# Kernel optimization log

Hardware: AMD Instinct MI355X
Metric: run time of the kernel (lower is better)

Reference implementation:

```python
import jax, jax.numpy as jnp
import numpy as np

VOCAB, EMBED, HIDDEN, N_CLASSES = 50257, 128, 256, 2
B = S = 512  # must be equal: the original module only runs when x.size(0)==x.size(1)


def gru_layer(x_seq, Wih, Whh, bih, bhh):
    """PyTorch-equation GRU over time axis 0. x_seq: (T, N, E) -> (T, N, H)."""
    T, N, _ = x_seq.shape
    H = Whh.shape[1]
    xi = x_seq @ Wih.T + bih  # precompute input projections for all steps: (T, N, 3H)

    def step(h, xi_t):
        gh = h @ Whh.T + bhh
        xr, xz, xn = jnp.split(xi_t, 3, axis=-1)
        hr, hz, hn = jnp.split(gh, 3, axis=-1)
        r = jax.nn.sigmoid(xr + hr)
        z = jax.nn.sigmoid(xz + hz)
        n = jnp.tanh(xn + r * hn)
        h_new = (1.0 - z) * n + z * h
        return h_new, h_new

    h0 = jnp.zeros((N, H), dtype=x_seq.dtype)
    _, ys = jax.lax.scan(step, h0, xi)
    return ys


def setup_inputs() -> dict:
    key = jax.random.key(0)
    ks = jax.random.split(key, 12)
    sc = 0.05
    return {
        "x": jax.random.randint(ks[0], (B, S), 0, VOCAB),
        "embed_table": jax.random.normal(ks[1], (VOCAB, EMBED), jnp.float32) * sc,
        "Wih0": jax.random.normal(ks[2], (3 * HIDDEN, EMBED), jnp.float32) * sc,
        "Whh0": jax.random.normal(ks[3], (3 * HIDDEN, HIDDEN), jnp.float32) * sc,
        "bih0": jax.random.normal(ks[4], (3 * HIDDEN,), jnp.float32) * sc,
        "bhh0": jax.random.normal(ks[5], (3 * HIDDEN,), jnp.float32) * sc,
        "Wih1": jax.random.normal(ks[6], (3 * HIDDEN, HIDDEN), jnp.float32) * sc,
        "Whh1": jax.random.normal(ks[7], (3 * HIDDEN, HIDDEN), jnp.float32) * sc,
        "bih1": jax.random.normal(ks[8], (3 * HIDDEN,), jnp.float32) * sc,
        "bhh1": jax.random.normal(ks[9], (3 * HIDDEN,), jnp.float32) * sc,
        "W_out": jax.random.normal(ks[10], (N_CLASSES, HIDDEN), jnp.float32) * sc,
        "b_out": jax.random.normal(ks[11], (N_CLASSES,), jnp.float32) * sc,
    }


def reference(x, embed_table, Wih0, Whh0, bih0, bhh0, Wih1, Whh1, bih1, bhh1, W_out, b_out):
    emb = embed_table[x]                 # (B, S, E)
    # nn.GRU default batch_first=False: dim 0 (=B) is TIME, dim 1 (=S) is batch.
    y = gru_layer(emb, Wih0, Whh0, bih0, bhh0)   # (B, S, H)
    y = gru_layer(y, Wih1, Whh1, bih1, bhh1)     # (B, S, H)
    h_t = y[:, -1, :]                    # (B, H)
    # self.dropout(h_t) in the original discards its result -> no-op.
    logit = h_t @ W_out.T + b_out        # (B, n_classes)
    return logit
```

## Files before the change

kernel.cpp:

```cpp
#include <hip/hip_runtime.h>
#include <hip/hip_fp16.h>

typedef _Float16 f16x2 __attribute__((ext_vector_type(2)));
typedef _Float16 half8 __attribute__((ext_vector_type(8)));

#define TS  512
#define HID 256
#define G3  768
#define EMB 128
#define NB1 8
#define RPB 96
#define CTL 767
#define BSZ 8

__device__ __forceinline__ float sigmoidf_(float x){ return 1.0f/(1.0f+__expf(-x)); }
__device__ __forceinline__ float tanhf_(float x){
  float e = __expf(-2.0f*fabsf(x));
  float t = (1.0f-e)/(1.0f+e);
  return copysignf(t,x);
}

__global__ __launch_bounds__(256) void xi0_kernel(const int* __restrict__ x,
    const float* __restrict__ emb_tab, const float* __restrict__ Wih0,
    const float* __restrict__ bih0, float* __restrict__ xi0)
{
  __shared__ float embs[8][EMB];
  __shared__ int idx8[8];
  int tid = threadIdx.x;
  int t0  = blockIdx.x * 8;
  if (tid < 8) idx8[tid] = x[(t0 + tid)*512 + 511];
  __syncthreads();
  for (int i = tid; i < 8*EMB; i += 256){
    int q = i >> 7, r = i & 127;
    embs[q][r] = emb_tab[(long)idx8[q]*EMB + r];
  }
  __syncthreads();
  for (int g = 0; g < 3; g++){
    int j = g*256 + tid;
    float b = bih0[j];
    float acc[8];
    #pragma unroll
    for (int u=0;u<8;u++) acc[u]=b;
    const float4* wrow = (const float4*)(Wih0 + (long)j*EMB);
    #pragma unroll 8
    for (int m=0;m<EMB/4;m++){
      float4 w = wrow[m];
      #pragma unroll
      for (int u=0;u<8;u++){
        acc[u] += w.x*embs[u][4*m+0] + w.y*embs[u][4*m+1]
                + w.z*embs[u][4*m+2] + w.w*embs[u][4*m+3];
      }
    }
    #pragma unroll
    for (int u=0;u<8;u++) xi0[(long)(t0+u)*G3 + j] = acc[u];
  }
}

#define SHUF(V,A,B) __builtin_shufflevector(V,V,A,B)
#define WR32(X) X(0,0) X(0,1) X(0,2) X(0,3) X(1,0) X(1,1) X(1,2) X(1,3) \
                X(2,0) X(2,1) X(2,2) X(2,3) X(3,0) X(3,1) X(3,2) X(3,3) \
                X(4,0) X(4,1) X(4,2) X(4,3) X(5,0) X(5,1) X(5,2) X(5,3) \
                X(6,0) X(6,1) X(6,2) X(6,3) X(7,0) X(7,1) X(7,2) X(7,3)

template<int MODE>
__device__ __forceinline__ void rec_layer(const float* __restrict__ Whh,
    const float* __restrict__ bhh, const float* __restrict__ xi,
    _Float16* __restrict__ h16out, float* __restrict__ f32out,
    unsigned* __restrict__ flagB, unsigned* __restrict__ cntB,
    _Float16 (*hbuf)[8*40], float* gh, float* bhhL)
{
  int tid = threadIdx.x;
  int g   = tid >> 3;
  int o   = tid & 7;

#define WDECL(I,C) half8 w##I##_##C;
  WR32(WDECL)
#define WLOAD(I,C) { \
    const float4* p_ = (const float4*)(Whh + (long)(8*g+(I))*HID + 32*o + 8*(C)); \
    float4 u_ = p_[0], v_ = p_[1]; \
    w##I##_##C = (half8){(_Float16)u_.x,(_Float16)u_.y,(_Float16)u_.z,(_Float16)u_.w, \
                         (_Float16)v_.x,(_Float16)v_.y,(_Float16)v_.z,(_Float16)v_.w}; }
  WR32(WLOAD)

  float hprev = 0.f;
  float xr=0.f, xz=0.f, xn=0.f;
  bhhL[tid] = bhh[tid];
  if (tid < 80) ((half8*)hbuf)[tid] = (half8)(_Float16)0;

  if (MODE == 1 && tid == CTL){
    while (__hip_atomic_load(&cntB[0], __ATOMIC_RELAXED, __HIP_MEMORY_SCOPE_AGENT) < NB1)
      __builtin_amdgcn_s_sleep(1);
    __threadfence();
  }
  __syncthreads();
  if (tid < HID){
    xr = xi[tid]; xz = xi[HID+tid]; xn = xi[2*HID+tid];
  }

  for (int t = 0; t < TS; t++){
    if (MODE == 1 && tid == CTL && ((t+1) & (BSZ-1)) == 0 && t+1 < TS){
      unsigned b = (unsigned)(t+1) >> 3;
      while (__hip_atomic_load(&cntB[b], __ATOMIC_RELAXED, __HIP_MEMORY_SCOPE_AGENT) < NB1)
        __builtin_amdgcn_s_sleep(1);
      __threadfence();
    }

    const half8* hp = (const half8*)(&hbuf[t & 1][o*40]);
    float a0=0.f,a1=0.f,a2=0.f,a3=0.f,a4=0.f,a5=0.f,a6=0.f,a7=0.f;
#define DOT1(I,C,HV) \
    a##I = __builtin_amdgcn_fdot2(SHUF(w##I##_##C,0,1), SHUF(HV,0,1), a##I, false); \
    a##I = __builtin_amdgcn_fdot2(SHUF(w##I##_##C,2,3), SHUF(HV,2,3), a##I, false); \
    a##I = __builtin_amdgcn_fdot2(SHUF(w##I##_##C,4,5), SHUF(HV,4,5), a##I, false); \
    a##I = __builtin_amdgcn_fdot2(SHUF(w##I##_##C,6,7), SHUF(HV,6,7), a##I, false);
#define DOTCHUNK(C) { half8 hv = hp[C]; \
    DOT1(0,C,hv) DOT1(1,C,hv) DOT1(2,C,hv) DOT1(3,C,hv) \
    DOT1(4,C,hv) DOT1(5,C,hv) DOT1(6,C,hv) DOT1(7,C,hv) }
    DOTCHUNK(0) DOTCHUNK(1) DOTCHUNK(2) DOTCHUNK(3)

    bool b0 = o & 1, b1 = o & 2, b2 = o & 4;
    float s, r_;
    s = b0 ? a0 : a1; r_ = __shfl_xor(s, 1, 64); float c0 = (b0 ? a1 : a0) + r_;
    s = b0 ? a2 : a3; r_ = __shfl_xor(s, 1, 64); float c1 = (b0 ? a3 : a2) + r_;
    s = b0 ? a4 : a5; r_ = __shfl_xor(s, 1, 64); float c2 = (b0 ? a5 : a4) + r_;
    s = b0 ? a6 : a7; r_ = __shfl_xor(s, 1, 64); float c3 = (b0 ? a7 : a6) + r_;
    s = b1 ? c0 : c1; r_ = __shfl_xor(s, 2, 64); float d0 = (b1 ? c1 : c0) + r_;
    s = b1 ? c2 : c3; r_ = __shfl_xor(s, 2, 64); float d1 = (b1 ? c3 : c2) + r_;
    s = b2 ? d0 : d1; r_ = __shfl_xor(s, 4, 64); float e  = (b2 ? d1 : d0) + r_;
    gh[tid] = e;
    __syncthreads();

    if (tid < HID){
      float r = sigmoidf_(xr + bhhL[tid] + gh[tid]);
      float z = sigmoidf_(xz + bhhL[HID+tid] + gh[HID+tid]);
      float n = tanhf_(xn + r*(gh[2*HID+tid] + bhhL[2*HID+tid]));
      float hnew = (1.0f - z)*n + z*hprev;
      hprev = hnew;
      if (MODE == 1) f32out[(long)t*HID + tid] = hnew;
      float partner = __shfl_xor(hnew, 1, 64);
      if ((tid & 1) == 0){
        f16x2 p; p.x = (_Float16)hnew; p.y = (_Float16)partner;
        *(f16x2*)(&hbuf[(t+1)&1][(tid>>5)*40 + (tid&31)]) = p;
        if (MODE == 0) *(f16x2*)(h16out + (long)t*HID + tid) = p;
      }
      if (t+1 < TS){
        const float* xp = xi + (long)(t+1)*G3;
        xr = xp[tid]; xz = xp[HID+tid]; xn = xp[2*HID+tid];
      }
    }
    __syncthreads();
    if (MODE == 0 && tid == CTL && ((t+1) & (BSZ-1)) == 0){
      __threadfence();
      __hip_atomic_store(&flagB[t >> 3], 1u, __ATOMIC_RELEASE, __HIP_MEMORY_SCOPE_AGENT);
    }
  }
}

__device__ __forceinline__ void xi1_stage(const float* __restrict__ Wih1,
    const float* __restrict__ bih1, const _Float16* __restrict__ h16,
    float* __restrict__ xi1, unsigned* __restrict__ flagB,
    unsigned* __restrict__ cntB, int slice)
{
  int tid = threadIdx.x;
  int r = tid >> 3, o = tid & 7;
  int row = slice*RPB + r;
  half8 w0,w1,w2,w3;
  {
    const float4* wp = (const float4*)(Wih1 + (long)row*HID + o*32);
    float4 p0=wp[0],p1=wp[1],p2=wp[2],p3=wp[3],p4=wp[4],p5=wp[5],p6=wp[6],p7=wp[7];
    w0 = (half8){(_Float16)p0.x,(_Float16)p0.y,(_Float16)p0.z,(_Float16)p0.w,
                 (_Float16)p1.x,(_Float16)p1.y,(_Float16)p1.z,(_Float16)p1.w};
    w1 = (half8){(_Float16)p2.x,(_Float16)p2.y,(_Float16)p2.z,(_Float16)p2.w,
                 (_Float16)p3.x,(_Float16)p3.y,(_Float16)p3.z,(_Float16)p3.w};
    w2 = (half8){(_Float16)p4.x,(_Float16)p4.y,(_Float16)p4.z,(_Float16)p4.w,
                 (_Float16)p5.x,(_Float16)p5.y,(_Float16)p5.z,(_Float16)p5.w};
    w3 = (half8){(_Float16)p6.x,(_Float16)p6.y,(_Float16)p6.z,(_Float16)p6.w,
                 (_Float16)p7.x,(_Float16)p7.y,(_Float16)p7.z,(_Float16)p7.w};
  }
  float bias = bih1[row];

  for (int b = 0; b < TS/BSZ; b++){
    if (tid == 0){
      while (__hip_atomic_load(&flagB[b], __ATOMIC_RELAXED, __HIP_MEMORY_SCOPE_AGENT) == 0u)
        __builtin_amdgcn_s_sleep(1);
      __threadfence();
    }
    __syncthreads();
    #pragma unroll 4
    for (int u = 0; u < BSZ; u++){
      int t = b*BSZ + u;
      const half8* hp = (const half8*)(h16 + (long)t*HID + o*32);
      half8 h0 = hp[0], h1 = hp[1], h2 = hp[2], h3 = hp[3];
      float acc = 0.f;
#define XDOT(W,H) \
      acc = __builtin_amdgcn_fdot2(SHUF(W,0,1), SHUF(H,0,1), acc, false); \
      acc = __builtin_amdgcn_fdot2(SHUF(W,2,3), SHUF(H,2,3), acc, false); \
      acc = __builtin_amdgcn_fdot2(SHUF(W,4,5), SHUF(H,4,5), acc, false); \
      acc = __builtin_amdgcn_fdot2(SHUF(W,6,7), SHUF(H,6,7), acc, false);
      XDOT(w0,h0) XDOT(w1,h1) XDOT(w2,h2) XDOT(w3,h3)
      acc += __shfl_xor(acc, 1, 64);
      acc += __shfl_xor(acc, 2, 64);
      acc += __shfl_xor(acc, 4, 64);
      if (o == 0) xi1[(long)t*G3 + row] = acc + bias;
    }
    __syncthreads();
    if (tid == 0){
      __threadfence();
      atomicAdd(&cntB[b], 1u);
    }
  }
}

__global__ __launch_bounds__(768, 3)
__attribute__((amdgpu_max_num_work_groups(10, 1, 1)))
void pipe_kernel(
    const float* __restrict__ Whh0, const float* __restrict__ bhh0,
    const float* __restrict__ xi0,
    const float* __restrict__ Wih1, const float* __restrict__ bih1,
    const float* __restrict__ Whh1, const float* __restrict__ bhh1,
    _Float16* __restrict__ h1f16, float* __restrict__ xi1,
    float* __restrict__ h2, unsigned* __restrict__ flagB,
    unsigned* __restrict__ cntB)
{
  __shared__ __align__(16) _Float16 hbuf[2][8*40];
  __shared__ float gh[G3];
  __shared__ float bhhL[G3];
  int bid = blockIdx.x;
  if (bid == 0)
    rec_layer<0>(Whh0, bhh0, xi0, h1f16, nullptr, flagB, cntB, hbuf, gh, bhhL);
  else if (bid == 9)
    rec_layer<1>(Whh1, bhh1, xi1, nullptr, h2, flagB, cntB, hbuf, gh, bhhL);
  else
    xi1_stage(Wih1, bih1, h1f16, xi1, flagB, cntB, bid - 1);
}

__global__ __launch_bounds__(1024) void logits_kernel(const float* __restrict__ h2,
    const float* __restrict__ Wout, const float* __restrict__ bout,
    float* __restrict__ out)
{
  __shared__ __align__(16) float wsm[2*HID];
  __shared__ float bs[2];
  int tid = threadIdx.x;
  if (tid < 2*HID) wsm[tid] = Wout[tid];
  if (tid < 2)     bs[tid]  = bout[tid];
  __syncthreads();
  int t = tid >> 1, c = tid & 1;
  const float4* hr = (const float4*)(h2 + (long)t*HID);
  const float4* wr = (const float4*)(wsm + c*HID);
  float acc = bs[c];
  #pragma unroll 8
  for (int m=0;m<HID/4;m++){
    float4 h = hr[m]; float4 wv = wr[m];
    acc += h.x*wv.x + h.y*wv.y + h.z*wv.z + h.w*wv.w;
  }
  out[tid] = acc;
}

extern "C" void kernel_launch(void* const* d_in, const int* in_sizes, int n_in,
                              void* d_out, int out_size, void* d_ws, size_t ws_size,
                              hipStream_t stream)
{
  const int*   x    = (const int*)  d_in[0];
  const float* emb  = (const float*)d_in[1];
  const float* Wih0 = (const float*)d_in[2];
  const float* Whh0 = (const float*)d_in[3];
  const float* bih0 = (const float*)d_in[4];
  const float* bhh0 = (const float*)d_in[5];
  const float* Wih1 = (const float*)d_in[6];
  const float* Whh1 = (const float*)d_in[7];
  const float* bih1 = (const float*)d_in[8];
  const float* bhh1 = (const float*)d_in[9];
  const float* Wout = (const float*)d_in[10];
  const float* bout = (const float*)d_in[11];
  float* out = (float*)d_out;

  char* ws = (char*)d_ws;
  float*     xi0   = (float*)(ws);
  float*     xi1   = (float*)(ws + 1572864);
  _Float16*  h1f16 = (_Float16*)(ws + 3145728);
  float*     h2    = (float*)(ws + 3407872);
  unsigned*  flagB = (unsigned*)(ws + 3932160);
  unsigned*  cntB  = (unsigned*)(ws + 3934208);

  hipMemsetAsync(ws + 3932160, 0, 4096, stream);
  xi0_kernel<<<64, 256, 0, stream>>>(x, emb, Wih0, bih0, xi0);
  pipe_kernel<<<10, 768, 0, stream>>>(Whh0, bhh0, xi0, Wih1, bih1,
                                      Whh1, bhh1, h1f16, xi1, h2, flagB, cntB);
  logits_kernel<<<1, 1024, 0, stream>>>(h2, Wout, bout, out);
}
```

Baseline: 856.6 us.

## Offload recurrent weight rows from registers to LDS and pre-converted global tails

Keeps only 3 of 8 Whh row slices per thread in registers. Three more are stored as fp16 in a large LDS buffer, and two are pre-converted to fp16 by a new prep kernel and read from global memory each timestep. The goal is to relieve register pressure (possible spills) in the serial recurrent loop. The cost is extra LDS and global loads on the latency-critical per-step path and a large LDS footprint.

```diff
diff --git a/kernel.cpp b/kernel.cpp
--- a/kernel.cpp
+++ b/kernel.cpp
@@ -56,31 +56,68 @@
   }
 }
 
+__global__ __launch_bounds__(768) void prep_tails(const float* __restrict__ W0,
+    const float* __restrict__ W1, _Float16* __restrict__ D)
+{
+  int tid = threadIdx.x;
+  const float* W = blockIdx.x ? W1 : W0;
+  _Float16* Dp = D + (long)blockIdx.x*G3*64 + (long)tid*64;
+  int g = tid >> 3, o = tid & 7;
+  const float4* s3 = (const float4*)(W + (long)(8*g+3)*HID + 32*o);
+  const float4* s7 = (const float4*)(W + (long)(8*g+7)*HID + 32*o);
+  #pragma unroll
+  for (int c = 0; c < 4; c++){
+    float4 u = s3[2*c], v = s3[2*c+1];
+    *(half8*)(Dp + c*8) = (half8){(_Float16)u.x,(_Float16)u.y,(_Float16)u.z,(_Float16)u.w,
+                                  (_Float16)v.x,(_Float16)v.y,(_Float16)v.z,(_Float16)v.w};
+  }
+  #pragma unroll
+  for (int c = 0; c < 4; c++){
+    float4 u = s7[2*c], v = s7[2*c+1];
+    *(half8*)(Dp + 32 + c*8) = (half8){(_Float16)u.x,(_Float16)u.y,(_Float16)u.z,(_Float16)u.w,
+                                       (_Float16)v.x,(_Float16)v.y,(_Float16)v.z,(_Float16)v.w};
+  }
+}
+
 #define SHUF(V,A,B) __builtin_shufflevector(V,V,A,B)
-#define WR32(X) X(0,0) X(0,1) X(0,2) X(0,3) X(1,0) X(1,1) X(1,2) X(1,3) \
-                X(2,0) X(2,1) X(2,2) X(2,3) X(3,0) X(3,1) X(3,2) X(3,3) \
-                X(4,0) X(4,1) X(4,2) X(4,3) X(5,0) X(5,1) X(5,2) X(5,3) \
-                X(6,0) X(6,1) X(6,2) X(6,3) X(7,0) X(7,1) X(7,2) X(7,3)
+#define WR12(X) X(0,0) X(0,1) X(0,2) X(0,3) X(1,0) X(1,1) X(1,2) X(1,3) \
+                X(2,0) X(2,1) X(2,2) X(2,3)
 
 template<int MODE>
 __device__ __forceinline__ void rec_layer(const float* __restrict__ Whh,
     const float* __restrict__ bhh, const float* __restrict__ xi,
+    const _Float16* __restrict__ wtail,
     _Float16* __restrict__ h16out, float* __restrict__ f32out,
     unsigned* __restrict__ flagB, unsigned* __restrict__ cntB,
-    _Float16 (*hbuf)[8*40], float* gh, float* bhhL)
+    _Float16 (*hbuf)[8*40], float* gh, float* bhhL, _Float16* lws)
 {
   int tid = threadIdx.x;
   int g   = tid >> 3;
   int o   = tid & 7;
 
 #define WDECL(I,C) half8 w##I##_##C;
-  WR32(WDECL)
+  WR12(WDECL)
 #define WLOAD(I,C) { \
     const float4* p_ = (const float4*)(Whh + (long)(8*g+(I))*HID + 32*o + 8*(C)); \
     float4 u_ = p_[0], v_ = p_[1]; \
     w##I##_##C = (half8){(_Float16)u_.x,(_Float16)u_.y,(_Float16)u_.z,(_Float16)u_.w, \
                          (_Float16)v_.x,(_Float16)v_.y,(_Float16)v_.z,(_Float16)v_.w}; }
-  WR32(WLOAD)
+  WR12(WLOAD)
+
+  {
+    _Float16* myl = lws + tid*100;
+    #pragma unroll
+    for (int I = 0; I < 3; I++){
+      const float4* s = (const float4*)(Whh + (long)(8*g+4+I)*HID + 32*o);
+      #pragma unroll
+      for (int C = 0; C < 4; C++){
+        float4 u = s[2*C], v = s[2*C+1];
+        *(half8*)(myl + I*32 + C*8) =
+          (half8){(_Float16)u.x,(_Float16)u.y,(_Float16)u.z,(_Float16)u.w,
+                  (_Float16)v.x,(_Float16)v.y,(_Float16)v.z,(_Float16)v.w};
+      }
+    }
+  }
 
   float hprev = 0.f;
   float xr=0.f, xz=0.f, xn=0.f;
@@ -96,6 +133,9 @@
   if (tid < HID){
     xr = xi[tid]; xz = xi[HID+tid]; xn = xi[2*HID+tid];
   }
+
+  const _Float16* lb = lws + tid*100;
+  const half8*    tb = (const half8*)(wtail + (long)tid*64);
 
   for (int t = 0; t < TS; t++){
     if (MODE == 1 && tid == CTL && ((t+1) & (BSZ-1)) == 0 && t+1 < TS){
@@ -107,14 +147,21 @@
 
     const half8* hp = (const half8*)(&hbuf[t & 1][o*40]);
     float a0=0.f,a1=0.f,a2=0.f,a3=0.f,a4=0.f,a5=0.f,a6=0.f,a7=0.f;
-#define DOT1(I,C,HV) \
-    a##I = __builtin_amdgcn_fdot2(SHUF(w##I##_##C,0,1), SHUF(HV,0,1), a##I, false); \
-    a##I = __builtin_amdgcn_fdot2(SHUF(w##I##_##C,2,3), SHUF(HV,2,3), a##I, false); \
-    a##I = __builtin_amdgcn_fdot2(SHUF(w##I##_##C,4,5), SHUF(HV,4,5), a##I, false); \
-    a##I = __builtin_amdgcn_fdot2(SHUF(w##I##_##C,6,7), SHUF(HV,6,7), a##I, false);
-#define DOTCHUNK(C) { half8 hv = hp[C]; \
-    DOT1(0,C,hv) DOT1(1,C,hv) DOT1(2,C,hv) DOT1(3,C,hv) \
-    DOT1(4,C,hv) DOT1(5,C,hv) DOT1(6,C,hv) DOT1(7,C,hv) }
+#define DOTV(A,W,H) \
+    A = __builtin_amdgcn_fdot2(SHUF(W,0,1), SHUF(H,0,1), A, false); \
+    A = __builtin_amdgcn_fdot2(SHUF(W,2,3), SHUF(H,2,3), A, false); \
+    A = __builtin_amdgcn_fdot2(SHUF(W,4,5), SHUF(H,4,5), A, false); \
+    A = __builtin_amdgcn_fdot2(SHUF(W,6,7), SHUF(H,6,7), A, false);
+#define DOTCHUNK(C) { \
+    half8 hv = hp[C]; \
+    half8 t3 = tb[C]; \
+    half8 t7 = tb[4+(C)]; \
+    half8 l4 = *(const half8*)(lb +      (C)*8); \
+    half8 l5 = *(const half8*)(lb + 32 + (C)*8); \
+    half8 l6 = *(const half8*)(lb + 64 + (C)*8); \
+    DOTV(a0, w0_##C, hv) DOTV(a1, w1_##C, hv) DOTV(a2, w2_##C, hv) \
+    DOTV(a3, t3, hv) DOTV(a4, l4, hv) DOTV(a5, l5, hv) DOTV(a6, l6, hv) \
+    DOTV(a7, t7, hv) }
     DOTCHUNK(0) DOTCHUNK(1) DOTCHUNK(2) DOTCHUNK(3)
 
     bool b0 = o & 1, b1 = o & 2, b2 = o & 4;
@@ -211,24 +258,25 @@
 }
 
 __global__ __launch_bounds__(768, 3)
-__attribute__((amdgpu_max_num_work_groups(10, 1, 1)))
 void pipe_kernel(
     const float* __restrict__ Whh0, const float* __restrict__ bhh0,
     const float* __restrict__ xi0,
     const float* __restrict__ Wih1, const float* __restrict__ bih1,
     const float* __restrict__ Whh1, const float* __restrict__ bhh1,
+    const _Float16* __restrict__ wtails,
     _Float16* __restrict__ h1f16, float* __restrict__ xi1,
     float* __restrict__ h2, unsigned* __restrict__ flagB,
     unsigned* __restrict__ cntB)
 {
+  __shared__ __align__(16) _Float16 lws[G3*100];
   __shared__ __align__(16) _Float16 hbuf[2][8*40];
   __shared__ float gh[G3];
   __shared__ float bhhL[G3];
   int bid = blockIdx.x;
   if (bid == 0)
-    rec_layer<0>(Whh0, bhh0, xi0, h1f16, nullptr, flagB, cntB, hbuf, gh, bhhL);
+    rec_layer<0>(Whh0, bhh0, xi0, wtails, h1f16, nullptr, flagB, cntB, hbuf, gh, bhhL, lws);
   else if (bid == 9)
-    rec_layer<1>(Whh1, bhh1, xi1, nullptr, h2, flagB, cntB, hbuf, gh, bhhL);
+    rec_layer<1>(Whh1, bhh1, xi1, wtails + (long)G3*64, nullptr, h2, flagB, cntB, hbuf, gh, bhhL, lws);
   else
     xi1_stage(Wih1, bih1, h1f16, xi1, flagB, cntB, bid - 1);
 }
@@ -274,16 +322,19 @@
   float* out = (float*)d_out;
 
   char* ws = (char*)d_ws;
-  float*     xi0   = (float*)(ws);
-  float*     xi1   = (float*)(ws + 1572864);
-  _Float16*  h1f16 = (_Float16*)(ws + 3145728);
-  float*     h2    = (float*)(ws + 3407872);
-  unsigned*  flagB = (unsigned*)(ws + 3932160);
-  unsigned*  cntB  = (unsigned*)(ws + 3934208);
+  float*     xi0    = (float*)(ws);
+  float*     xi1    = (float*)(ws + 1572864);
+  _Float16*  h1f16  = (_Float16*)(ws + 3145728);
+  float*     h2     = (float*)(ws + 3407872);
+  unsigned*  flagB  = (unsigned*)(ws + 3932160);
+  unsigned*  cntB   = (unsigned*)(ws + 3934208);
+  _Float16*  wtails = (_Float16*)(ws + 3936256);
 
   hipMemsetAsync(ws + 3932160, 0, 4096, stream);
-  xi0_kernel<<<64, 256, 0, stream>>>(x, emb, Wih0, bih0, xi0);
+  prep_tails <<<2, 768, 0, stream>>>(Whh0, Whh1, wtails);
+  xi0_kernel <<<64, 256, 0, stream>>>(x, emb, Wih0, bih0, xi0);
   pipe_kernel<<<10, 768, 0, stream>>>(Whh0, bhh0, xi0, Wih1, bih1,
-                                      Whh1, bhh1, h1f16, xi1, h2, flagB, cntB);
+                                      Whh1, bhh1, wtails, h1f16, xi1, h2,
+                                      flagB, cntB);
   logits_kernel<<<1, 1024, 0, stream>>>(h2, Wout, bout, out);
 }
```

Measured after the change: 2.563 ms. 2.99x slower.
